# Kernel tuning notes

Hardware: AMD Instinct MI355X
Metric: run time of the kernel (lower is better)

## Reference

```python
import jax, jax.numpy as jnp
import numpy as np

N_NODES = 100000
N_EDGES = 1600000
NODE_DIM = 64
HIDDEN = 256
OUT_DIM = 64
BN_EPS = 1e-5


def setup_inputs() -> dict:
    key = jax.random.key(0)
    ks = jax.random.split(key, 6)
    h = jax.random.normal(ks[0], (N_NODES, NODE_DIM), dtype=jnp.float32)
    W1 = jax.random.normal(ks[1], (NODE_DIM, HIDDEN), dtype=jnp.float32) * 0.1
    b1 = jnp.zeros((HIDDEN,), dtype=jnp.float32)
    W2 = jax.random.normal(ks[2], (HIDDEN, OUT_DIM), dtype=jnp.float32) * 0.1
    b2 = jnp.zeros((OUT_DIM,), dtype=jnp.float32)
    gamma = jnp.ones((OUT_DIM,), dtype=jnp.float32)
    beta = jnp.zeros((OUT_DIM,), dtype=jnp.float32)
    src = jax.random.randint(ks[3], (N_EDGES,), 0, N_NODES, dtype=jnp.int32)
    dst = jax.random.randint(ks[4], (N_EDGES,), 0, N_NODES, dtype=jnp.int32)
    return {"h": h, "W1": W1, "b1": b1, "W2": W2, "b2": b2,
            "gamma": gamma, "beta": beta, "src": src, "dst": dst}


def reference(h, W1, b1, W2, b2, gamma, beta, src, dst):
    # --- mean aggregation over incoming neighbors (DGL update_all) ---
    # mailbox mean == segment_sum(h[src]) / in_degree(dst), zero for isolated nodes
    agg_sum = jax.ops.segment_sum(h[src], dst, num_segments=N_NODES)  # [N, d]
    deg = jax.ops.segment_sum(jnp.ones((src.shape[0],), h.dtype), dst,
                              num_segments=N_NODES)
    agg = agg_sum / jnp.clip(deg, 1.0, None)[:, None]
    x = agg + h  # GIN combine: aggregated msg + self feature
    # --- 2-layer MLP with relu, then final relu (node_update_fn) ---
    x = jax.nn.relu(x @ W1 + b1)
    x = x @ W2 + b2
    x = jax.nn.relu(x)
    # --- BatchNorm1d over node (batch) dimension, training-mode stats ---
    mean = jnp.mean(x, axis=0)
    var = jnp.var(x, axis=0)  # biased variance, as torch BN training
    x = (x - mean) * jax.lax.rsqrt(var + BN_EPS) * gamma + beta
    return x
```

## Files before the change

kernel.cpp:

```cpp
#include <hip/hip_runtime.h>

#define N_NODES 100000
#define N_EDGES 1600000
#define DIM     64
#define HID     256
#define BN_EPS  1e-5f

#define NBUCK   391
#define RSTRIDE 392
#define SCHUNK  3125
#define SBLK    512
#define MAXB    6144

#define XBROWS  100032
#define NGP     782
#define MLPGRID 256
#define MAXIT   4

typedef short bf16x8 __attribute__((ext_vector_type(8)));
typedef float f32x4  __attribute__((ext_vector_type(4)));


__device__ __forceinline__ unsigned short f2bf(float x) {
    union { __bf16 b; unsigned short u; } cv;
    cv.b = (__bf16)x;
    return cv.u;
}
__device__ __forceinline__ unsigned pk2(float a, float b) {
    return (unsigned)f2bf(a) | ((unsigned)f2bf(b) << 16);
}

#define WAITV(N) asm volatile("s_waitcnt vmcnt(" #N ")" ::: "memory")

__device__ __forceinline__ void stage_issue(const unsigned short* gsrc,
                                            unsigned short* ldst) {
    __builtin_amdgcn_global_load_lds(
        (const __attribute__((address_space(1))) void*)gsrc,
        (__attribute__((address_space(3))) void*)ldst, 16, 0, 0);
    __builtin_amdgcn_global_load_lds(
        (const __attribute__((address_space(1))) void*)(gsrc + 512),
        (__attribute__((address_space(3))) void*)(ldst + 512), 16, 0, 0);
}

__global__ __launch_bounds__(1024) void kA_scatter(const int* __restrict__ src,
                                                   const int* __restrict__ dst,
                                                   const float* __restrict__ h,
                                                   const float* __restrict__ W1,
                                                   const float* __restrict__ W2,
                                                   unsigned int* __restrict__ ebuf,
                                                   int* __restrict__ runoff,
                                                   unsigned short* __restrict__ w1t,
                                                   unsigned short* __restrict__ w2t,
                                                   unsigned short* __restrict__ xb,
                                                   unsigned short* __restrict__ hb,
                                                   int* __restrict__ statsbar) {
    __shared__ int hist[NBUCK];
    __shared__ int ebase[NBUCK];
    __shared__ int sc[512];
    __shared__ unsigned int stage[SCHUNK];
    const int t = threadIdx.x;
    const int e0 = blockIdx.x * SCHUNK;
    const int n = SCHUNK;

    for (int i = t; i < NBUCK; i += 1024) hist[i] = 0;
    __syncthreads();
    for (int i = t; i < n; i += 1024)
        atomicAdd(&hist[dst[e0 + i] >> 8], 1);
    __syncthreads();

    if (t < 512) sc[t] = (t < NBUCK) ? hist[t] : 0;
    __syncthreads();
    for (int off = 1; off < 512; off <<= 1) {
        int add = (t < 512 && t >= off) ? sc[t - off] : 0;
        __syncthreads();
        if (t < 512) sc[t] += add;
        __syncthreads();
    }
    if (t < NBUCK) {
        int ex = sc[t] - hist[t];
        ebase[t] = ex;
        runoff[blockIdx.x * RSTRIDE + t] = ex;
    }
    if (t == 0) runoff[blockIdx.x * RSTRIDE + NBUCK] = n;
    if (t < NBUCK) hist[t] = 0;
    __syncthreads();

    for (int i = t; i < n; i += 1024) {
        int d = dst[e0 + i];
        int s = src[e0 + i];
        int b = d >> 8;
        int r = atomicAdd(&hist[b], 1);
        stage[ebase[b] + r] = ((unsigned int)s << 8) | (unsigned int)(d & 255);
    }
    __syncthreads();
    for (int i = t; i < n; i += 1024)
        ebuf[e0 + i] = stage[i];

    for (int i = blockIdx.x * 1024 + t; i < 800000; i += SBLK * 1024) {
        int e = i * 8;
        float4 f0 = *(const float4*)&h[e];
        float4 f1 = *(const float4*)&h[e + 4];
        uint4 o;
        o.x = pk2(f0.x, f0.y);
        o.y = pk2(f0.z, f0.w);
        o.z = pk2(f1.x, f1.y);
        o.w = pk2(f1.z, f1.w);
        *(uint4*)&hb[e] = o;
    }
    int id = blockIdx.x * 1024 + t;
    if (id < 16384) {
        int nn = id >> 6, k = id & 63;
        int dstp = (nn << 6) + ((((k >> 3) ^ (nn & 7))) << 3) + (k & 7);
        w1t[dstp] = f2bf(W1[k * 256 + nn]);
    } else if (id < 32768) {
        int i2 = id - 16384;
        int d = i2 >> 8, k2 = i2 & 255;
        int dstp = (d << 8) + ((((k2 >> 3) ^ (d & 7))) << 3) + (k2 & 7);
        w2t[dstp] = f2bf(W2[k2 * 64 + d]);
    } else if (id < 34816) {
        xb[100000 * 64 + (id - 32768)] = 0;
    }
    if (blockIdx.x == 34 && t < 256) statsbar[t] = 0;
}

__global__ __launch_bounds__(1024) void kB_fused(const unsigned int* __restrict__ ebuf,
                                                 const int* __restrict__ runoff,
                                                 const unsigned short* __restrict__ hb,
                                                 unsigned short* __restrict__ xb) {
    __shared__ int runbase[SBLK + 1];
    __shared__ int sc[SBLK];
    __shared__ int cnt[256];
    __shared__ int off[256];
    __shared__ unsigned int stage2[MAXB];
    __shared__ unsigned int sout[MAXB];
    const int t = threadIdx.x;
    const int b = blockIdx.x;

    int rl = 0, rs = 0;
    if (t < SBLK) {
        int s = runoff[t * RSTRIDE + b];
        int e = runoff[t * RSTRIDE + b + 1];
        rs = t * SCHUNK + s;
        rl = e - s;
        sc[t] = rl;
    }
    if (t < 256) cnt[t] = 0;
    __syncthreads();
    for (int o = 1; o < SBLK; o <<= 1) {
        int add = (t < SBLK && t >= o) ? sc[t - o] : 0;
        __syncthreads();
        if (t < SBLK) sc[t] += add;
        __syncthreads();
    }
    if (t == 0) runbase[SBLK] = sc[SBLK - 1];
    __syncthreads();
    const int total = min(runbase[SBLK], MAXB);

    if (t < SBLK && rl > 0) {
        int base = sc[t] - rl;
        int lim = min(rl, MAXB - base);
        for (int k = 0; k < lim; ++k) {
            unsigned int v = ebuf[rs + k];
            stage2[base + k] = v;
            atomicAdd(&cnt[v & 255u], 1);
        }
    }
    __syncthreads();

    int c0 = (t < 256) ? cnt[t] : 0;
    if (t < 256) sc[t] = c0;
    __syncthreads();
    for (int o = 1; o < 256; o <<= 1) {
        int add = (t < 256 && t >= o) ? sc[t - o] : 0;
        __syncthreads();
        if (t < 256) sc[t] += add;
        __syncthreads();
    }
    if (t < 256) { off[t] = sc[t] - c0; cnt[t] = 0; }
    __syncthreads();

    for (int idx = t; idx < total; idx += 1024) {
        unsigned int v = stage2[idx];
        int node = (int)(v & 255u);
        int r = atomicAdd(&cnt[node], 1);
        sout[off[node] + r] = v >> 8;
    }
    __syncthreads();

    const int g = t >> 3, c = t & 7;
    const unsigned short* hc = hb + c * 8;
    const int gn0 = b * 256;
#pragma unroll
    for (int pass = 0; pass < 2; ++pass) {
        int nloc = pass * 128 + g;
        int gnode = gn0 + nloc;
        if (gnode >= N_NODES) continue;
        const int o0 = off[nloc];
        const int dg = cnt[nloc];
        float a0 = 0.f, a1 = 0.f, a2 = 0.f, a3 = 0.f;
        float a4 = 0.f, a5 = 0.f, a6 = 0.f, a7 = 0.f;
        int j = 0;
        for (; j + 1 < dg; j += 2) {
            int i0 = (int)sout[o0 + j];
            int i1 = (int)sout[o0 + j + 1];
            uint4 v0 = *(const uint4*)&hc[(size_t)i0 * 64];
            uint4 v1 = *(const uint4*)&hc[(size_t)i1 * 64];
            a0 += __uint_as_float(v0.x << 16); a1 += __uint_as_float(v0.x & 0xffff0000u);
            a2 += __uint_as_float(v0.y << 16); a3 += __uint_as_float(v0.y & 0xffff0000u);
            a4 += __uint_as_float(v0.z << 16); a5 += __uint_as_float(v0.z & 0xffff0000u);
            a6 += __uint_as_float(v0.w << 16); a7 += __uint_as_float(v0.w & 0xffff0000u);
            a0 += __uint_as_float(v1.x << 16); a1 += __uint_as_float(v1.x & 0xffff0000u);
            a2 += __uint_as_float(v1.y << 16); a3 += __uint_as_float(v1.y & 0xffff0000u);
            a4 += __uint_as_float(v1.z << 16); a5 += __uint_as_float(v1.z & 0xffff0000u);
            a6 += __uint_as_float(v1.w << 16); a7 += __uint_as_float(v1.w & 0xffff0000u);
        }
        if (j < dg) {
            int i0 = (int)sout[o0 + j];
            uint4 v0 = *(const uint4*)&hc[(size_t)i0 * 64];
            a0 += __uint_as_float(v0.x << 16); a1 += __uint_as_float(v0.x & 0xffff0000u);
            a2 += __uint_as_float(v0.y << 16); a3 += __uint_as_float(v0.y & 0xffff0000u);
            a4 += __uint_as_float(v0.z << 16); a5 += __uint_as_float(v0.z & 0xffff0000u);
            a6 += __uint_as_float(v0.w << 16); a7 += __uint_as_float(v0.w & 0xffff0000u);
        }
        const float inv = 1.0f / (float)max(dg, 1);
        uint4 ov = *(const uint4*)&hc[(size_t)gnode * 64];
        float x0 = fmaf(a0, inv, __uint_as_float(ov.x << 16));
        float x1 = fmaf(a1, inv, __uint_as_float(ov.x & 0xffff0000u));
        float x2 = fmaf(a2, inv, __uint_as_float(ov.y << 16));
        float x3 = fmaf(a3, inv, __uint_as_float(ov.y & 0xffff0000u));
        float x4 = fmaf(a4, inv, __uint_as_float(ov.z << 16));
        float x5 = fmaf(a5, inv, __uint_as_float(ov.z & 0xffff0000u));
        float x6 = fmaf(a6, inv, __uint_as_float(ov.w << 16));
        float x7 = fmaf(a7, inv, __uint_as_float(ov.w & 0xffff0000u));
        uint4 o;
        o.x = pk2(x0, x1);
        o.y = pk2(x2, x3);
        o.z = pk2(x4, x5);
        o.w = pk2(x6, x7);
        *(uint4*)&xb[(size_t)gnode * 64 + ((c ^ (gnode & 7)) << 3)] = o;
    }
}

__device__ __forceinline__ void mlp_tile(const unsigned short* sXw,
                                         const unsigned short* sW1,
                                         const unsigned short* sW2,
                                         unsigned short* sHw,
                                         const float* sB1,
                                         int l15, int g4, int s7,
                                         f32x4 oacc[4]) {
    bf16x8 xf0 = *(const bf16x8*)&sXw[l15 * 64 + ((g4 ^ s7) << 3)];
    bf16x8 xf1 = *(const bf16x8*)&sXw[l15 * 64 + (((g4 + 4) ^ s7) << 3)];
#pragma unroll
    for (int dt = 0; dt < 4; ++dt) oacc[dt] = (f32x4){0.f, 0.f, 0.f, 0.f};

#pragma unroll
    for (int p = 0; p < 4; ++p) {
#pragma unroll
        for (int nt2 = 0; nt2 < 4; ++nt2) {
            const int n0 = p * 64 + nt2 * 16;
            f32x4 hacc = (f32x4){0.f, 0.f, 0.f, 0.f};
            bf16x8 wf0 = *(const bf16x8*)&sW1[(n0 + l15) * 64 + ((g4 ^ s7) << 3)];
            bf16x8 wf1 = *(const bf16x8*)&sW1[(n0 + l15) * 64 + (((g4 + 4) ^ s7) << 3)];
            hacc = __builtin_amdgcn_mfma_f32_16x16x32_bf16(wf0, xf0, hacc, 0, 0, 0);
            hacc = __builtin_amdgcn_mfma_f32_16x16x32_bf16(wf1, xf1, hacc, 0, 0, 0);
            float4 bq = *(const float4*)&sB1[n0 + g4 * 4];
            ushort2 pkl, pkh;
            unsigned plo = pk2(fmaxf(hacc[0] + bq.x, 0.f),
                               fmaxf(hacc[1] + bq.y, 0.f));
            unsigned phi = pk2(fmaxf(hacc[2] + bq.z, 0.f),
                               fmaxf(hacc[3] + bq.w, 0.f));
            int qh = nt2 * 2 + (g4 >> 1);
            uint2 pk = {plo, phi};
            *(uint2*)&sHw[l15 * 64 + ((qh ^ s7) << 3) + ((g4 & 1) << 2)] = pk;
        }
#pragma unroll
        for (int s2 = 0; s2 < 2; ++s2) {
            bf16x8 a2 = *(const bf16x8*)&sHw[l15 * 64 + (((s2 * 4 + g4) ^ s7) << 3)];
#pragma unroll
            for (int dt = 0; dt < 4; ++dt) {
                int q = p * 8 + s2 * 4 + g4;
                bf16x8 w2f = *(const bf16x8*)&sW2[(dt * 16 + l15) * 256 + ((q ^ s7) << 3)];
                oacc[dt] = __builtin_amdgcn_mfma_f32_16x16x32_bf16(a2, w2f, oacc[dt], 0, 0, 0);
            }
        }
    }
}

__global__ __launch_bounds__(512, 2) void k_mlpf(const unsigned short* __restrict__ xb,
                                                 const unsigned short* __restrict__ w1t,
                                                 const unsigned short* __restrict__ w2t,
                                                 const float* __restrict__ b1,
                                                 const float* __restrict__ b2,
                                                 const float* __restrict__ gamma,
                                                 const float* __restrict__ beta,
                                                 float* __restrict__ stats,
                                                 int* __restrict__ bar,
                                                 float* __restrict__ out,
                                                 float* __restrict__ dump) {
    __shared__ unsigned short sW1[256 * 64];
    __shared__ unsigned short sW2[64 * 256];
    __shared__ unsigned short sH[8][16 * 64];
    __shared__ unsigned short sX[8][2][16 * 64];
    __shared__ float sB1[256];
    const int t = threadIdx.x;
    const int lane = t & 63;
    const int w = t >> 6;
    const int l15 = lane & 15;
    const int g4 = lane >> 4;
    const int s7 = l15 & 7;
    const int bid = blockIdx.x;

    for (int i = t; i < 2048; i += 512)
        *(uint4*)&sW1[i * 8] = *(const uint4*)&w1t[i * 8];
    for (int i = t; i < 2048; i += 512)
        *(uint4*)&sW2[i * 8] = *(const uint4*)&w2t[i * 8];
    if (t < 256) sB1[t] = b1[t];
    __syncthreads();

    float b2v[4];
#pragma unroll
    for (int dt = 0; dt < 4; ++dt) b2v[dt] = b2[dt * 16 + l15];

    float lsum[4] = {0.f, 0.f, 0.f, 0.f};
    float lsq[4]  = {0.f, 0.f, 0.f, 0.f};
    f32x4 osave[MAXIT][4];

    int cur = 0;
    {
        int r0 = min(bid * 128 + w * 16, XBROWS - 16);
        stage_issue(xb + (size_t)r0 * 64 + lane * 8, &sX[w][0][0]);
    }
#pragma unroll
    for (int it = 0; it < MAXIT; ++it) {
        int gp = bid + it * MLPGRID;
        int gpn = gp + MLPGRID; if (gpn >= NGP) gpn = gp;
        int r0n = min(gpn * 128 + w * 16, XBROWS - 16);
        stage_issue(xb + (size_t)r0n * 64 + lane * 8, &sX[w][cur ^ 1][0]);
        WAITV(2);
        __builtin_amdgcn_sched_barrier(0);
        const int row0 = gp * 128 + w * 16;
        if (gp < NGP && row0 < XBROWS) {
            f32x4 oacc[4];
            mlp_tile(&sX[w][cur][0], sW1, sW2, &sH[w][0], sB1, l15, g4, s7, oacc);
#pragma unroll
            for (int dt = 0; dt < 4; ++dt) {
#pragma unroll
                for (int r = 0; r < 4; ++r) {
                    float val = fmaxf(oacc[dt][r] + b2v[dt], 0.f);
                    osave[it][dt][r] = val;
                    int mabs = row0 + g4 * 4 + r;
                    if (mabs < N_NODES) {
                        lsum[dt] += val;
                        lsq[dt] += val * val;
                    }
                }
            }
        }
        cur ^= 1;
    }

    __syncthreads();
    float* sred = (float*)&sW1[0];
#pragma unroll
    for (int dt = 0; dt < 4; ++dt) {
        sred[t * 8 + dt] = lsum[dt];
        sred[t * 8 + 4 + dt] = lsq[dt];
    }
    __syncthreads();
    if (t < 128) {
        int issq = (t >= 64) ? 4 : 0;
        int d = t & 63;
        int dt = d >> 4, dl = d & 15;
        float acc = 0.f;
        for (int i = 0; i < 32; ++i) acc += sred[(dl + 16 * i) * 8 + issq + dt];
        atomicAdd(&stats[(issq ? 64 : 0) + d], acc);
    }

    __syncthreads();
    if (t == 0) {
        __hip_atomic_fetch_add(bar, 1, __ATOMIC_ACQ_REL, __HIP_MEMORY_SCOPE_AGENT);
        while (__hip_atomic_load(bar, __ATOMIC_ACQUIRE, __HIP_MEMORY_SCOPE_AGENT)
               < MLPGRID)
            __builtin_amdgcn_s_sleep(4);
    }
    __syncthreads();

    float scv[4], shv[4];
    const float inv_n = 1.0f / (float)N_NODES;
#pragma unroll
    for (int dt = 0; dt < 4; ++dt) {
        int d = dt * 16 + l15;
        float sm = __hip_atomic_load(&stats[d], __ATOMIC_RELAXED,
                                     __HIP_MEMORY_SCOPE_AGENT);
        float sq = __hip_atomic_load(&stats[64 + d], __ATOMIC_RELAXED,
                                     __HIP_MEMORY_SCOPE_AGENT);
        float m = sm * inv_n;
        float v = sq * inv_n - m * m;
        float sc = gamma[d] * rsqrtf(v + BN_EPS);
        scv[dt] = sc;
        shv[dt] = beta[d] - m * sc;
    }

#pragma unroll
    for (int it = 0; it < MAXIT; ++it) {
        int gp = bid + it * MLPGRID;
        const int row0 = gp * 128 + w * 16;
        if (gp >= NGP || row0 >= XBROWS) continue;
        float* sHf = (float*)&sH[w][0];
#pragma unroll
        for (int hh = 0; hh < 2; ++hh) {
            asm volatile("" ::: "memory");
            if ((g4 >> 1) == hh) {
#pragma unroll
                for (int dt = 0; dt < 4; ++dt) {
#pragma unroll
                    for (int r = 0; r < 4; ++r) {
                        float val = fmaf(osave[it][dt][r], scv[dt], shv[dt]);
                        sHf[((g4 & 1) * 4 + r) * 64 + dt * 16 + l15] = val;
                    }
                }
            }
            asm volatile("" ::: "memory");
#pragma unroll
            for (int j = 0; j < 2; ++j) {
                int rl = j * 4 + (lane >> 4);
                int rg = row0 + hh * 8 + rl;
                float4 v = *(const float4*)&sHf[rl * 64 + (lane & 15) * 4];
                float* dstp = (rg < N_NODES)
                    ? &out[(size_t)rg * 64 + (lane & 15) * 4]
                    : &dump[lane * 4];
                *(float4*)dstp = v;
            }
        }
    }
}

extern "C" void kernel_launch(void* const* d_in, const int* in_sizes, int n_in,
                              void* d_out, int out_size, void* d_ws, size_t ws_size,
                              hipStream_t stream) {
    const float* h     = (const float*)d_in[0];
    const float* W1    = (const float*)d_in[1];
    const float* b1    = (const float*)d_in[2];
    const float* W2    = (const float*)d_in[3];
    const float* b2    = (const float*)d_in[4];
    const float* gamma = (const float*)d_in[5];
    const float* beta  = (const float*)d_in[6];
    const int*   src   = (const int*)d_in[7];
    const int*   dst   = (const int*)d_in[8];

    int* wsi = (int*)d_ws;
    float*          stats   = (float*)wsi;
    int*            bar     = wsi + 128;
    int*            statsbar = wsi;
    int*            runoff  = wsi + 256;
    float*          dump    = (float*)(wsi + 256);
    unsigned short* w1t     = (unsigned short*)(wsi + 200960);
    unsigned short* w2t     = (unsigned short*)(wsi + 209152);
    unsigned short* xb      = (unsigned short*)(wsi + 217344);
    unsigned int*   ebuf    = (unsigned int*)(wsi + 3418368);
    unsigned short* hb      = (unsigned short*)(wsi + 5018368);
    float*          out     = (float*)d_out;

    kA_scatter<<<SBLK, 1024, 0, stream>>>(src, dst, h, W1, W2, ebuf, runoff,
                                          w1t, w2t, xb, hb, statsbar);
    kB_fused<<<NBUCK, 1024, 0, stream>>>(ebuf, runoff, hb, xb);
    k_mlpf<<<MLPGRID, 512, 0, stream>>>(xb, w1t, w2t, b1, b2, gamma, beta,
                                        stats, bar, out, dump);
}
```

Measured before the change: 172.2 us.

## Split edge staging across all threads, prefetch gathers, widen MLP blocks to 1024

The bucket kernel now stages each run's edges with two threads instead of one, so all 1024 threads do the global-to-shared copy. The neighbor gather loop is software-pipelined so the next pair of feature rows loads while the current pair accumulates. The fused MLP kernel moves from 512-thread blocks with double-buffered staging to 1024-thread blocks covering 256 rows per tile, with single-buffered staging and a full wait. That drops the overlap of the X-tile load with compute and raises per-block register and LDS pressure, while removing iterations from the grid-stride loop.

```diff
diff --git a/kernel.cpp b/kernel.cpp
--- a/kernel.cpp
+++ b/kernel.cpp
@@ -13,9 +13,9 @@
 #define MAXB    6144
 
 #define XBROWS  100032
-#define NGP     782
+#define NT      391
 #define MLPGRID 256
-#define MAXIT   4
+#define MAXIT   2
 
 typedef short bf16x8 __attribute__((ext_vector_type(8)));
 typedef float f32x4  __attribute__((ext_vector_type(4)));
@@ -127,7 +127,7 @@
                                                  const int* __restrict__ runoff,
                                                  const unsigned short* __restrict__ hb,
                                                  unsigned short* __restrict__ xb) {
-    __shared__ int runbase[SBLK + 1];
+    __shared__ int runstart_s[SBLK];
     __shared__ int sc[SBLK];
     __shared__ int cnt[256];
     __shared__ int off[256];
@@ -136,11 +136,11 @@
     const int t = threadIdx.x;
     const int b = blockIdx.x;
 
-    int rl = 0, rs = 0;
+    int rl = 0;
     if (t < SBLK) {
         int s = runoff[t * RSTRIDE + b];
         int e = runoff[t * RSTRIDE + b + 1];
-        rs = t * SCHUNK + s;
+        runstart_s[t] = t * SCHUNK + s;
         rl = e - s;
         sc[t] = rl;
     }
@@ -152,16 +152,23 @@
         if (t < SBLK) sc[t] += add;
         __syncthreads();
     }
-    if (t == 0) runbase[SBLK] = sc[SBLK - 1];
-    __syncthreads();
-    const int total = min(runbase[SBLK], MAXB);
-
-    if (t < SBLK && rl > 0) {
-        int base = sc[t] - rl;
-        int lim = min(rl, MAXB - base);
-        for (int k = 0; k < lim; ++k) {
-            unsigned int v = ebuf[rs + k];
-            stage2[base + k] = v;
+    const int total = min(sc[SBLK - 1], MAXB);
+    __syncthreads();
+
+    {
+        const int r = t & 511;
+        const int hf = t >> 9;
+        int prev = (r == 0) ? 0 : sc[r - 1];
+        int rlr = sc[r] - prev;
+        int h0 = (rlr + 1) >> 1;
+        int st = hf ? h0 : 0;
+        int en = hf ? rlr : h0;
+        int rs0 = runstart_s[r];
+        for (int k = st; k < en; ++k) {
+            int pos = prev + k;
+            if (pos >= MAXB) break;
+            unsigned int v = ebuf[rs0 + k];
+            stage2[pos] = v;
             atomicAdd(&cnt[v & 255u], 1);
         }
     }
@@ -199,24 +206,35 @@
         const int dg = cnt[nloc];
         float a0 = 0.f, a1 = 0.f, a2 = 0.f, a3 = 0.f;
         float a4 = 0.f, a5 = 0.f, a6 = 0.f, a7 = 0.f;
-        int j = 0;
-        for (; j + 1 < dg; j += 2) {
-            int i0 = (int)sout[o0 + j];
-            int i1 = (int)sout[o0 + j + 1];
-            uint4 v0 = *(const uint4*)&hc[(size_t)i0 * 64];
-            uint4 v1 = *(const uint4*)&hc[(size_t)i1 * 64];
-            a0 += __uint_as_float(v0.x << 16); a1 += __uint_as_float(v0.x & 0xffff0000u);
-            a2 += __uint_as_float(v0.y << 16); a3 += __uint_as_float(v0.y & 0xffff0000u);
-            a4 += __uint_as_float(v0.z << 16); a5 += __uint_as_float(v0.z & 0xffff0000u);
-            a6 += __uint_as_float(v0.w << 16); a7 += __uint_as_float(v0.w & 0xffff0000u);
-            a0 += __uint_as_float(v1.x << 16); a1 += __uint_as_float(v1.x & 0xffff0000u);
-            a2 += __uint_as_float(v1.y << 16); a3 += __uint_as_float(v1.y & 0xffff0000u);
-            a4 += __uint_as_float(v1.z << 16); a5 += __uint_as_float(v1.z & 0xffff0000u);
-            a6 += __uint_as_float(v1.w << 16); a7 += __uint_as_float(v1.w & 0xffff0000u);
-        }
-        if (j < dg) {
-            int i0 = (int)sout[o0 + j];
-            uint4 v0 = *(const uint4*)&hc[(size_t)i0 * 64];
+        const int npair = dg >> 1;
+        uint4 p0, p1;
+        if (npair > 0) {
+            int i0 = (int)sout[o0];
+            int i1 = (int)sout[o0 + 1];
+            p0 = *(const uint4*)&hc[(size_t)i0 * 64];
+            p1 = *(const uint4*)&hc[(size_t)i1 * 64];
+        }
+        for (int q = 0; q < npair; ++q) {
+            uint4 c0v = p0, c1v = p1;
+            int j2 = (q + 1) * 2;
+            if (q + 1 < npair) {
+                int ia = (int)sout[o0 + j2];
+                int ib = (int)sout[o0 + j2 + 1];
+                p0 = *(const uint4*)&hc[(size_t)ia * 64];
+                p1 = *(const uint4*)&hc[(size_t)ib * 64];
+            }
+            a0 += __uint_as_float(c0v.x << 16); a1 += __uint_as_float(c0v.x & 0xffff0000u);
+            a2 += __uint_as_float(c0v.y << 16); a3 += __uint_as_float(c0v.y & 0xffff0000u);
+            a4 += __uint_as_float(c0v.z << 16); a5 += __uint_as_float(c0v.z & 0xffff0000u);
+            a6 += __uint_as_float(c0v.w << 16); a7 += __uint_as_float(c0v.w & 0xffff0000u);
+            a0 += __uint_as_float(c1v.x << 16); a1 += __uint_as_float(c1v.x & 0xffff0000u);
+            a2 += __uint_as_float(c1v.y << 16); a3 += __uint_as_float(c1v.y & 0xffff0000u);
+            a4 += __uint_as_float(c1v.z << 16); a5 += __uint_as_float(c1v.z & 0xffff0000u);
+            a6 += __uint_as_float(c1v.w << 16); a7 += __uint_as_float(c1v.w & 0xffff0000u);
+        }
+        if (dg & 1) {
+            int il = (int)sout[o0 + dg - 1];
+            uint4 v0 = *(const uint4*)&hc[(size_t)il * 64];
             a0 += __uint_as_float(v0.x << 16); a1 += __uint_as_float(v0.x & 0xffff0000u);
             a2 += __uint_as_float(v0.y << 16); a3 += __uint_as_float(v0.y & 0xffff0000u);
             a4 += __uint_as_float(v0.z << 16); a5 += __uint_as_float(v0.z & 0xffff0000u);
@@ -264,7 +282,6 @@
             hacc = __builtin_amdgcn_mfma_f32_16x16x32_bf16(wf0, xf0, hacc, 0, 0, 0);
             hacc = __builtin_amdgcn_mfma_f32_16x16x32_bf16(wf1, xf1, hacc, 0, 0, 0);
             float4 bq = *(const float4*)&sB1[n0 + g4 * 4];
-            ushort2 pkl, pkh;
             unsigned plo = pk2(fmaxf(hacc[0] + bq.x, 0.f),
                                fmaxf(hacc[1] + bq.y, 0.f));
             unsigned phi = pk2(fmaxf(hacc[2] + bq.z, 0.f),
@@ -286,21 +303,21 @@
     }
 }
 
-__global__ __launch_bounds__(512, 2) void k_mlpf(const unsigned short* __restrict__ xb,
-                                                 const unsigned short* __restrict__ w1t,
-                                                 const unsigned short* __restrict__ w2t,
-                                                 const float* __restrict__ b1,
-                                                 const float* __restrict__ b2,
-                                                 const float* __restrict__ gamma,
-                                                 const float* __restrict__ beta,
-                                                 float* __restrict__ stats,
-                                                 int* __restrict__ bar,
-                                                 float* __restrict__ out,
-                                                 float* __restrict__ dump) {
+__global__ __launch_bounds__(1024, 1) void k_mlpf(const unsigned short* __restrict__ xb,
+                                                  const unsigned short* __restrict__ w1t,
+                                                  const unsigned short* __restrict__ w2t,
+                                                  const float* __restrict__ b1,
+                                                  const float* __restrict__ b2,
+                                                  const float* __restrict__ gamma,
+                                                  const float* __restrict__ beta,
+                                                  float* __restrict__ stats,
+                                                  int* __restrict__ bar,
+                                                  float* __restrict__ out,
+                                                  float* __restrict__ dump) {
     __shared__ unsigned short sW1[256 * 64];
     __shared__ unsigned short sW2[64 * 256];
-    __shared__ unsigned short sH[8][16 * 64];
-    __shared__ unsigned short sX[8][2][16 * 64];
+    __shared__ unsigned short sH[16][16 * 64];
+    __shared__ unsigned short sX[16][16 * 64];
     __shared__ float sB1[256];
     const int t = threadIdx.x;
     const int lane = t & 63;
@@ -310,9 +327,9 @@
     const int s7 = l15 & 7;
     const int bid = blockIdx.x;
 
-    for (int i = t; i < 2048; i += 512)
+    for (int i = t; i < 2048; i += 1024)
         *(uint4*)&sW1[i * 8] = *(const uint4*)&w1t[i * 8];
-    for (int i = t; i < 2048; i += 512)
+    for (int i = t; i < 2048; i += 1024)
         *(uint4*)&sW2[i * 8] = *(const uint4*)&w2t[i * 8];
     if (t < 256) sB1[t] = b1[t];
     __syncthreads();
@@ -325,23 +342,17 @@
     float lsq[4]  = {0.f, 0.f, 0.f, 0.f};
     f32x4 osave[MAXIT][4];
 
-    int cur = 0;
-    {
-        int r0 = min(bid * 128 + w * 16, XBROWS - 16);
-        stage_issue(xb + (size_t)r0 * 64 + lane * 8, &sX[w][0][0]);
-    }
 #pragma unroll
     for (int it = 0; it < MAXIT; ++it) {
         int gp = bid + it * MLPGRID;
-        int gpn = gp + MLPGRID; if (gpn >= NGP) gpn = gp;
-        int r0n = min(gpn * 128 + w * 16, XBROWS - 16);
-        stage_issue(xb + (size_t)r0n * 64 + lane * 8, &sX[w][cur ^ 1][0]);
-        WAITV(2);
+        int r0c = min(gp * 256 + w * 16, XBROWS - 16);
+        stage_issue(xb + (size_t)r0c * 64 + lane * 8, &sX[w][0]);
+        WAITV(0);
         __builtin_amdgcn_sched_barrier(0);
-        const int row0 = gp * 128 + w * 16;
-        if (gp < NGP && row0 < XBROWS) {
+        const int row0 = gp * 256 + w * 16;
+        if (gp < NT && row0 < XBROWS) {
             f32x4 oacc[4];
-            mlp_tile(&sX[w][cur][0], sW1, sW2, &sH[w][0], sB1, l15, g4, s7, oacc);
+            mlp_tile(&sX[w][0], sW1, sW2, &sH[w][0], sB1, l15, g4, s7, oacc);
 #pragma unroll
             for (int dt = 0; dt < 4; ++dt) {
 #pragma unroll
@@ -356,7 +367,6 @@
                 }
             }
         }
-        cur ^= 1;
     }
 
     __syncthreads();
@@ -372,7 +382,7 @@
         int d = t & 63;
         int dt = d >> 4, dl = d & 15;
         float acc = 0.f;
-        for (int i = 0; i < 32; ++i) acc += sred[(dl + 16 * i) * 8 + issq + dt];
+        for (int i = 0; i < 64; ++i) acc += sred[(dl + 16 * i) * 8 + issq + dt];
         atomicAdd(&stats[(issq ? 64 : 0) + d], acc);
     }
 
@@ -404,8 +414,8 @@
 #pragma unroll
     for (int it = 0; it < MAXIT; ++it) {
         int gp = bid + it * MLPGRID;
-        const int row0 = gp * 128 + w * 16;
-        if (gp >= NGP || row0 >= XBROWS) continue;
+        const int row0 = gp * 256 + w * 16;
+        if (gp >= NT || row0 >= XBROWS) continue;
         float* sHf = (float*)&sH[w][0];
 #pragma unroll
         for (int hh = 0; hh < 2; ++hh) {
@@ -449,21 +459,21 @@
     const int*   dst   = (const int*)d_in[8];
 
     int* wsi = (int*)d_ws;
-    float*          stats   = (float*)wsi;
-    int*            bar     = wsi + 128;
+    float*          stats    = (float*)wsi;
+    int*            bar      = wsi + 128;
     int*            statsbar = wsi;
-    int*            runoff  = wsi + 256;
-    float*          dump    = (float*)(wsi + 256);
-    unsigned short* w1t     = (unsigned short*)(wsi + 200960);
-    unsigned short* w2t     = (unsigned short*)(wsi + 209152);
-    unsigned short* xb      = (unsigned short*)(wsi + 217344);
-    unsigned int*   ebuf    = (unsigned int*)(wsi + 3418368);
-    unsigned short* hb      = (unsigned short*)(wsi + 5018368);
-    float*          out     = (float*)d_out;
+    int*            runoff   = wsi + 256;
+    float*          dump     = (float*)(wsi + 256);
+    unsigned short* w1t      = (unsigned short*)(wsi + 200960);
+    unsigned short* w2t      = (unsigned short*)(wsi + 209152);
+    unsigned short* xb       = (unsigned short*)(wsi + 217344);
+    unsigned int*   ebuf     = (unsigned int*)(wsi + 3418368);
+    unsigned short* hb       = (unsigned short*)(wsi + 5018368);
+    float*          out      = (float*)d_out;
 
     kA_scatter<<<SBLK, 1024, 0, stream>>>(src, dst, h, W1, W2, ebuf, runoff,
                                           w1t, w2t, xb, hb, statsbar);
     kB_fused<<<NBUCK, 1024, 0, stream>>>(ebuf, runoff, hb, xb);
-    k_mlpf<<<MLPGRID, 512, 0, stream>>>(xb, w1t, w2t, b1, b2, gamma, beta,
-                                        stats, bar, out, dump);
-}
+    k_mlpf<<<MLPGRID, 1024, 0, stream>>>(xb, w1t, w2t, b1, b2, gamma, beta,
+                                         stats, bar, out, dump);
+}
```

Measured after the change: 174.4 us. Within noise of the previous version (+1.3%).
